# Optimization experiments

Hardware: AMD Instinct MI355X
Metric: run time of the kernel (lower is better)

## Reference

```python
import jax, jax.numpy as jnp
import numpy as np

ALPHA = 0.25  # sparsity init kwarg


def setup_inputs() -> dict:
    key = jax.random.key(0)
    x = jax.random.uniform(key, (32, 256, 256, 16), dtype=jnp.float32)
    return {"x": x}


def reference(x):
    # Original TF code loops over every pixel i in H*W, slicing (B,1,C) and
    # calling force_sparsity, where p = reduce_mean over the WHOLE slice
    # (batch AND channel). Vectorized: p has shape (H, W).
    p = jnp.mean(x, axis=(0, 3))            # (H, W) per-pixel mean over B,C
    p_b = p[None, :, :, None]                # broadcast to (1, H, W, 1)
    beta = (1.0 - ALPHA) / (1.0 - p_b)
    le = p_b >= ALPHA                        # branch selector per pixel
    out = jnp.where(le,
                    x * ALPHA / p_b,
                    1.0 - beta * (1.0 - x))
    return out
```

## Files before the change

### kernel.cpp

```cpp
#include <hip/hip_runtime.h>


#define ALPHA 0.25f

typedef float v4f __attribute__((ext_vector_type(4)));

__global__ __launch_bounds__(256) void rescale_prob_mask_kernel(
    const float* __restrict__ x, float* __restrict__ out) {
  constexpr int ELEM_PER_B = 256 * 256 * 16;

  __shared__ float lds[32][256];

  const int tile = blockIdx.x;
  const int h    = tile >> 4;
  const int w0   = (tile & 15) << 4;
  const long tile_base_f = ((long)h * 256 + w0) * 16;

  const int t  = threadIdx.x;
  const int l  = t & 63;
  const int wv = t >> 6;

#pragma unroll
  for (int k = 0; k < 8; ++k) {
    const int b = 4 * k + wv;
    const float* src = x + tile_base_f + (long)b * ELEM_PER_B + l * 4;
    __builtin_amdgcn_global_load_lds(
        (const __attribute__((address_space(1))) unsigned int*)src,
        (__attribute__((address_space(3))) unsigned int*)&lds[b][0],
        16, 0, 0);
  }
  __syncthreads();

  const int j = l & 15;
  float4 v[8];
  float s = 0.0f;
#pragma unroll
  for (int k = 0; k < 8; ++k) {
    const int r = 4 * k + (l >> 4);
    v[k] = *(const float4*)&lds[r][wv * 64 + j * 4];
    s += (v[k].x + v[k].y) + (v[k].z + v[k].w);
  }
  s += __shfl_xor(s, 1);
  s += __shfl_xor(s, 2);
  s += __shfl_xor(s, 16);
  s += __shfl_xor(s, 32);
  const float p = s * (1.0f / 512.0f);

  float a, d;
  if (p >= ALPHA) {
    a = ALPHA / p;
    d = 0.0f;
  } else {
    const float beta = (1.0f - ALPHA) / (1.0f - p);
    a = beta;
    d = 1.0f - beta;
  }

#pragma unroll
  for (int k = 0; k < 8; ++k) {
    const int r = 4 * k + (l >> 4);
    v4f o;
    o.x = fmaf(a, v[k].x, d);
    o.y = fmaf(a, v[k].y, d);
    o.z = fmaf(a, v[k].z, d);
    o.w = fmaf(a, v[k].w, d);
    float* dst = out + tile_base_f + (long)r * ELEM_PER_B + (wv * 16 + j) * 4;
    __builtin_nontemporal_store(o, (v4f*)dst);
  }
}

extern "C" void kernel_launch(void* const* d_in, const int* in_sizes, int n_in,
                              void* d_out, int out_size, void* d_ws, size_t ws_size,
                              hipStream_t stream) {
  const float* x = (const float*)d_in[0];
  float* out = (float*)d_out;
  rescale_prob_mask_kernel<<<dim3(4096), dim3(256), 0, stream>>>(x, out);
}
```

Baseline: 241.1 us.

## Split fused reduce-and-rescale into separate reduction and apply kernels

Replaces the single LDS-staged kernel with a reduction kernel that computes per-pixel scale/offset pairs into workspace, followed by a streaming apply kernel. This aims to simplify memory access patterns and remove LDS staging and block synchronization. In exchange x is read twice from memory, adding traffic unless the second read hits cache, plus an extra launch.

```diff
diff --git a/kernel.cpp b/kernel.cpp
--- a/kernel.cpp
+++ b/kernel.cpp
@@ -5,45 +5,26 @@
 
 typedef float v4f __attribute__((ext_vector_type(4)));
 
-__global__ __launch_bounds__(256) void rescale_prob_mask_kernel(
-    const float* __restrict__ x, float* __restrict__ out) {
-  constexpr int ELEM_PER_B = 256 * 256 * 16;
+__global__ __launch_bounds__(256) void reduce_kernel(
+    const float* __restrict__ x, float2* __restrict__ ad) {
+  constexpr long ELEM_PER_B = 1L << 20;
 
-  __shared__ float lds[32][256];
+  const int t  = blockIdx.x * 256 + threadIdx.x;
+  const int hw = t >> 3;
+  const int cq = t & 3;
+  const int bh = (t >> 2) & 1;
 
-  const int tile = blockIdx.x;
-  const int h    = tile >> 4;
-  const int w0   = (tile & 15) << 4;
-  const long tile_base_f = ((long)h * 256 + w0) * 16;
+  const float* base = x + (long)hw * 16 + cq * 4 + (long)bh * 16 * ELEM_PER_B;
 
-  const int t  = threadIdx.x;
-  const int l  = t & 63;
-  const int wv = t >> 6;
-
-#pragma unroll
-  for (int k = 0; k < 8; ++k) {
-    const int b = 4 * k + wv;
-    const float* src = x + tile_base_f + (long)b * ELEM_PER_B + l * 4;
-    __builtin_amdgcn_global_load_lds(
-        (const __attribute__((address_space(1))) unsigned int*)src,
-        (__attribute__((address_space(3))) unsigned int*)&lds[b][0],
-        16, 0, 0);
-  }
-  __syncthreads();
-
-  const int j = l & 15;
-  float4 v[8];
   float s = 0.0f;
 #pragma unroll
-  for (int k = 0; k < 8; ++k) {
-    const int r = 4 * k + (l >> 4);
-    v[k] = *(const float4*)&lds[r][wv * 64 + j * 4];
-    s += (v[k].x + v[k].y) + (v[k].z + v[k].w);
+  for (int bi = 0; bi < 16; ++bi) {
+    const float4 v = *(const float4*)(base + (long)bi * ELEM_PER_B);
+    s += (v.x + v.y) + (v.z + v.w);
   }
   s += __shfl_xor(s, 1);
   s += __shfl_xor(s, 2);
-  s += __shfl_xor(s, 16);
-  s += __shfl_xor(s, 32);
+  s += __shfl_xor(s, 4);
   const float p = s * (1.0f / 512.0f);
 
   float a, d;
@@ -55,17 +36,31 @@
     a = beta;
     d = 1.0f - beta;
   }
+  if ((t & 7) == 0) ad[hw] = make_float2(a, d);
+}
+
+__global__ __launch_bounds__(256) void apply_kernel(
+    const float* __restrict__ x, const float2* __restrict__ ad,
+    float* __restrict__ out) {
+  constexpr long STRIDE_F4 = 2048L * 256;
+  constexpr int F4_PER_B_MASK = (1 << 18) - 1;
+
+  const long i = (long)blockIdx.x * 256 + threadIdx.x;
+  const int inb = (int)i & F4_PER_B_MASK;
+  const float2 adv = ad[inb >> 2];
+
+  const float4* __restrict__ xp = (const float4*)x + i;
+  v4f* __restrict__ op = (v4f*)out + i;
 
 #pragma unroll
-  for (int k = 0; k < 8; ++k) {
-    const int r = 4 * k + (l >> 4);
-    v4f o;
-    o.x = fmaf(a, v[k].x, d);
-    o.y = fmaf(a, v[k].y, d);
-    o.z = fmaf(a, v[k].z, d);
-    o.w = fmaf(a, v[k].w, d);
-    float* dst = out + tile_base_f + (long)r * ELEM_PER_B + (wv * 16 + j) * 4;
-    __builtin_nontemporal_store(o, (v4f*)dst);
+  for (int j = 0; j < 16; ++j) {
+    const float4 v = xp[j * STRIDE_F4];
+    v4f r;
+    r.x = fmaf(adv.x, v.x, adv.y);
+    r.y = fmaf(adv.x, v.y, adv.y);
+    r.z = fmaf(adv.x, v.z, adv.y);
+    r.w = fmaf(adv.x, v.w, adv.y);
+    __builtin_nontemporal_store(r, op + j * STRIDE_F4);
   }
 }
 
@@ -74,5 +69,8 @@
                               hipStream_t stream) {
   const float* x = (const float*)d_in[0];
   float* out = (float*)d_out;
-  rescale_prob_mask_kernel<<<dim3(4096), dim3(256), 0, stream>>>(x, out);
+  float2* ad = (float2*)d_ws;
+
+  reduce_kernel<<<dim3(2048), dim3(256), 0, stream>>>(x, ad);
+  apply_kernel<<<dim3(2048), dim3(256), 0, stream>>>(x, ad, out);
 }
```

After: 252.8 us. 4.9% more time.
